# Optimization experiments

Hardware: AMD Instinct MI355X
Metric: run time of the kernel (lower is better)

The kernel has to match this reference:

```python
import jax, jax.numpy as jnp
import numpy as np

B, C, IMG = 512, 3, 112


def setup_inputs() -> dict:
    key = jax.random.key(0)
    k0, k1, k2 = jax.random.split(key, 3)
    img = jax.random.normal(k0, (B, C, IMG, IMG), dtype=jnp.float32)
    # fc[0]: Linear(3*H*W -> 20); fc[3]: Linear(20 -> 6) init weight=0, bias=identity.
    # Use small random W2 so the warp is non-trivial (math identical regardless).
    W1 = jax.random.normal(k1, (C * IMG * IMG, 20), dtype=jnp.float32) * 0.005
    b1 = jnp.zeros((20,), dtype=jnp.float32)
    W2 = jax.random.normal(k2, (20, 6), dtype=jnp.float32) * 0.01
    b2 = jnp.array([1, 0, 0, 0, 1, 0], dtype=jnp.float32)
    return {"img": img, "W1": W1, "b1": b1, "W2": W2, "b2": b2}


def reference(img, W1, b1, W2, b2):
    Bn, Cn, H, W = img.shape
    h = jnp.tanh(img.reshape(Bn, -1) @ W1 + b1)            # [B, 20]
    theta = jnp.tanh(h @ W2 + b2).reshape(Bn, 2, 3)        # [B, 2, 3]

    # F.affine_grid, align_corners=False: pixel-center normalized coords
    xs = (2.0 * jnp.arange(W, dtype=jnp.float32) + 1.0) / W - 1.0
    ys = (2.0 * jnp.arange(H, dtype=jnp.float32) + 1.0) / H - 1.0
    gy, gx = jnp.meshgrid(ys, xs, indexing="ij")           # [H, W]
    base = jnp.stack([gx, gy, jnp.ones_like(gx)], axis=-1)  # [H, W, 3] -> (x, y, 1)
    grid = jnp.einsum("bij,hwj->bhwi", theta, base)        # [B, H, W, 2], (x, y)

    # F.grid_sample, bilinear, padding_mode='zeros', align_corners=False
    ix = ((grid[..., 0] + 1.0) * W - 1.0) * 0.5            # [B, H, W] src x
    iy = ((grid[..., 1] + 1.0) * H - 1.0) * 0.5            # [B, H, W] src y
    x0f = jnp.floor(ix); y0f = jnp.floor(iy)
    wx1 = ix - x0f; wx0 = 1.0 - wx1
    wy1 = iy - y0f; wy0 = 1.0 - wy1

    img_hwc = img.transpose(0, 2, 3, 1)                    # [B, H, W, C]
    bidx = jnp.arange(Bn)[:, None, None]

    def gather(xf, yf):
        valid = (xf >= 0) & (xf <= W - 1) & (yf >= 0) & (yf <= H - 1)
        xc = jnp.clip(xf, 0, W - 1).astype(jnp.int32)
        yc = jnp.clip(yf, 0, H - 1).astype(jnp.int32)
        v = img_hwc[bidx, yc, xc]                           # [B, H, W, C]
        return v * valid[..., None].astype(img.dtype)

    out = (gather(x0f, y0f) * (wx0 * wy0)[..., None]
           + gather(x0f + 1, y0f) * (wx1 * wy0)[..., None]
           + gather(x0f, y0f + 1) * (wx0 * wy1)[..., None]
           + gather(x0f + 1, y0f + 1) * (wx1 * wy1)[..., None])
    return out.transpose(0, 3, 1, 2)                       # [B, C, H, W]
```

## Files before the change

### kernel.cpp

```cpp
#include <hip/hip_runtime.h>
#include <math.h>

#define BATCH 512
#define CHAN 3
#define IMG 112
#define HW (IMG*IMG)
#define K_TOT (CHAN*HW)
#define NH 20
#define F4_TOT (K_TOT/4)
#define KT 4
#define F4_PER_TILE (F4_TOT/KT)
#define MB 4

__global__ __launch_bounds__(256, 2)
void gemm1_kernel(const float* __restrict__ img, const float* __restrict__ W1,
                  float* __restrict__ partial) {
    const int tid = threadIdx.x;
    const int kt  = blockIdx.x;
    const int b0  = blockIdx.y * MB;
    const long base = (long)b0 * K_TOT;

    float acc[MB][NH];
    #pragma unroll
    for (int i = 0; i < MB; ++i)
        #pragma unroll
        for (int n = 0; n < NH; ++n) acc[i][n] = 0.f;

    const int f4start = kt * F4_PER_TILE;
    const int f4end   = f4start + F4_PER_TILE;

    for (int f = f4start + tid; f < f4end; f += 256) {
        const int k = f * 4;
        float4 iv[MB];
        #pragma unroll
        for (int i = 0; i < MB; ++i)
            iv[i] = *reinterpret_cast<const float4*>(img + base + (long)i * K_TOT + k);

        #pragma unroll
        for (int j = 0; j < 4; ++j) {
            const float4* wr = reinterpret_cast<const float4*>(W1 + (long)(k + j) * NH);
            float4 wq[5];
            #pragma unroll
            for (int q = 0; q < 5; ++q) wq[q] = wr[q];
            const float* wf = reinterpret_cast<const float*>(wq);
            #pragma unroll
            for (int i = 0; i < MB; ++i) {
                const float xi = reinterpret_cast<const float*>(&iv[i])[j];
                #pragma unroll
                for (int n = 0; n < NH; ++n)
                    acc[i][n] = fmaf(xi, wf[n], acc[i][n]);
            }
        }
    }

    __shared__ float red[4][MB * NH];
    const int wave = tid >> 6, lane = tid & 63;
    #pragma unroll
    for (int i = 0; i < MB; ++i)
        #pragma unroll
        for (int n = 0; n < NH; ++n) {
            float v = acc[i][n];
            #pragma unroll
            for (int off = 32; off > 0; off >>= 1) v += __shfl_xor(v, off, 64);
            if (lane == 0) red[wave][i * NH + n] = v;
        }
    __syncthreads();
    if (tid < MB * NH) {
        float s = red[0][tid] + red[1][tid] + red[2][tid] + red[3][tid];
        const int i = tid / NH, n = tid - i * NH;
        partial[((long)kt * BATCH + (b0 + i)) * NH + n] = s;
    }
}

__global__ __launch_bounds__(256)
void theta_kernel(const float* __restrict__ partial, const float* __restrict__ b1,
                  const float* __restrict__ W2, const float* __restrict__ b2,
                  float* __restrict__ theta) {
    const int b = blockIdx.x * 256 + threadIdx.x;
    if (b >= BATCH) return;
    float h[NH];
    #pragma unroll
    for (int n = 0; n < NH; ++n) {
        float s = b1[n];
        #pragma unroll
        for (int kt = 0; kt < KT; ++kt)
            s += partial[((long)kt * BATCH + b) * NH + n];
        h[n] = tanhf(s);
    }
    #pragma unroll
    for (int j = 0; j < 6; ++j) {
        float s = b2[j];
        #pragma unroll
        for (int n = 0; n < NH; ++n) s = fmaf(h[n], W2[n * 6 + j], s);
        theta[b * 6 + j] = tanhf(s);
    }
}

__global__ __launch_bounds__(256)
void warp_kernel(const float* __restrict__ img, const float* __restrict__ theta,
                 float* __restrict__ out) {
    const int b   = blockIdx.y;
    const int pix = blockIdx.x * 256 + threadIdx.x;
    const int y = pix / IMG;
    const int x = pix - y * IMG;

    const float* t = theta + b * 6;
    const float xs = (2.f * x + 1.f) / (float)IMG - 1.f;
    const float ys = (2.f * y + 1.f) / (float)IMG - 1.f;
    const float gx = t[0] * xs + t[1] * ys + t[2];
    const float gy = t[3] * xs + t[4] * ys + t[5];

    const float ix = ((gx + 1.f) * (float)IMG - 1.f) * 0.5f;
    const float iy = ((gy + 1.f) * (float)IMG - 1.f) * 0.5f;

    const float x0f = floorf(ix), y0f = floorf(iy);
    const float wx1 = ix - x0f, wx0 = 1.f - wx1;
    const float wy1 = iy - y0f, wy0 = 1.f - wy1;
    const int x0 = (int)x0f, y0 = (int)y0f;
    const int x1 = x0 + 1, y1 = y0 + 1;

    const bool vx0 = (x0 >= 0) & (x0 <= IMG - 1);
    const bool vx1 = (x1 >= 0) & (x1 <= IMG - 1);
    const bool vy0 = (y0 >= 0) & (y0 <= IMG - 1);
    const bool vy1 = (y1 >= 0) & (y1 <= IMG - 1);
    const int cx0 = min(max(x0, 0), IMG - 1), cx1 = min(max(x1, 0), IMG - 1);
    const int cy0 = min(max(y0, 0), IMG - 1), cy1 = min(max(y1, 0), IMG - 1);

    const float w00 = (vx0 && vy0) ? wx0 * wy0 : 0.f;
    const float w10 = (vx1 && vy0) ? wx1 * wy0 : 0.f;
    const float w01 = (vx0 && vy1) ? wx0 * wy1 : 0.f;
    const float w11 = (vx1 && vy1) ? wx1 * wy1 : 0.f;

    const long ib = (long)b * CHAN * HW;
    const int o00 = cy0 * IMG + cx0, o10 = cy0 * IMG + cx1;
    const int o01 = cy1 * IMG + cx0, o11 = cy1 * IMG + cx1;
    #pragma unroll
    for (int c = 0; c < CHAN; ++c) {
        const float* p = img + ib + (long)c * HW;
        const float v = w00 * p[o00] + w10 * p[o10] + w01 * p[o01] + w11 * p[o11];
        out[ib + (long)c * HW + pix] = v;
    }
}

extern "C" void kernel_launch(void* const* d_in, const int* in_sizes, int n_in,
                              void* d_out, int out_size, void* d_ws, size_t ws_size,
                              hipStream_t stream) {
    const float* img = (const float*)d_in[0];
    const float* W1  = (const float*)d_in[1];
    const float* b1  = (const float*)d_in[2];
    const float* W2  = (const float*)d_in[3];
    const float* b2  = (const float*)d_in[4];
    float* out = (float*)d_out;

    float* partial = (float*)d_ws;
    float* theta   = partial + (long)KT * BATCH * NH;

    gemm1_kernel<<<dim3(KT, BATCH / MB), 256, 0, stream>>>(img, W1, partial);
    theta_kernel<<<dim3((BATCH + 255) / 256), 256, 0, stream>>>(partial, b1, W2, b2, theta);
    warp_kernel<<<dim3(HW / 256, BATCH), 256, 0, stream>>>(img, theta, out);
}
```

Baseline: 235.4 us.

## Split GEMM K into more tiles, parallelize theta per batch, vectorize warp output

The first GEMM splits K into 16 tiles instead of 4, so the grid has four times as many blocks, and the min-blocks launch bound is dropped. The theta kernel now uses one block per batch item, with threads spread over the hidden units and outputs and a shared-memory handoff between the two layers. The warp kernel has each thread compute four adjacent pixels and write them as float4 stores, which cuts thread count and store instructions. The costs are more partial sums to reduce and more registers per warp thread.

```diff
diff --git a/kernel.cpp b/kernel.cpp
--- a/kernel.cpp
+++ b/kernel.cpp
@@ -8,11 +8,11 @@
 #define K_TOT (CHAN*HW)
 #define NH 20
 #define F4_TOT (K_TOT/4)
-#define KT 4
+#define KT 16
 #define F4_PER_TILE (F4_TOT/KT)
 #define MB 4
 
-__global__ __launch_bounds__(256, 2)
+__global__ __launch_bounds__(256)
 void gemm1_kernel(const float* __restrict__ img, const float* __restrict__ W1,
                   float* __restrict__ partial) {
     const int tid = threadIdx.x;
@@ -72,73 +72,87 @@
     }
 }
 
-__global__ __launch_bounds__(256)
+__global__ __launch_bounds__(64)
 void theta_kernel(const float* __restrict__ partial, const float* __restrict__ b1,
                   const float* __restrict__ W2, const float* __restrict__ b2,
                   float* __restrict__ theta) {
-    const int b = blockIdx.x * 256 + threadIdx.x;
-    if (b >= BATCH) return;
-    float h[NH];
-    #pragma unroll
-    for (int n = 0; n < NH; ++n) {
-        float s = b1[n];
+    const int b = blockIdx.x;
+    const int t = threadIdx.x;
+    __shared__ float h[NH];
+    if (t < NH) {
+        float s = b1[t];
         #pragma unroll
         for (int kt = 0; kt < KT; ++kt)
-            s += partial[((long)kt * BATCH + b) * NH + n];
-        h[n] = tanhf(s);
+            s += partial[((long)kt * BATCH + b) * NH + t];
+        h[t] = tanhf(s);
     }
-    #pragma unroll
-    for (int j = 0; j < 6; ++j) {
-        float s = b2[j];
+    __syncthreads();
+    if (t < 6) {
+        float s = b2[t];
         #pragma unroll
-        for (int n = 0; n < NH; ++n) s = fmaf(h[n], W2[n * 6 + j], s);
-        theta[b * 6 + j] = tanhf(s);
+        for (int n = 0; n < NH; ++n) s = fmaf(h[n], W2[n * 6 + t], s);
+        theta[b * 6 + t] = tanhf(s);
     }
 }
 
+#define QUADS (HW/4)
 __global__ __launch_bounds__(256)
 void warp_kernel(const float* __restrict__ img, const float* __restrict__ theta,
                  float* __restrict__ out) {
-    const int b   = blockIdx.y;
-    const int pix = blockIdx.x * 256 + threadIdx.x;
-    const int y = pix / IMG;
-    const int x = pix - y * IMG;
+    const int b = blockIdx.y;
+    const int quad = blockIdx.x * 256 + threadIdx.x;
+    if (quad >= QUADS) return;
+    const int y  = quad / (IMG / 4);
+    const int x0 = (quad - y * (IMG / 4)) * 4;
 
     const float* t = theta + b * 6;
-    const float xs = (2.f * x + 1.f) / (float)IMG - 1.f;
+    const float t0 = t[0], t1 = t[1], t2 = t[2], t3 = t[3], t4 = t[4], t5 = t[5];
     const float ys = (2.f * y + 1.f) / (float)IMG - 1.f;
-    const float gx = t[0] * xs + t[1] * ys + t[2];
-    const float gy = t[3] * xs + t[4] * ys + t[5];
-
-    const float ix = ((gx + 1.f) * (float)IMG - 1.f) * 0.5f;
-    const float iy = ((gy + 1.f) * (float)IMG - 1.f) * 0.5f;
-
-    const float x0f = floorf(ix), y0f = floorf(iy);
-    const float wx1 = ix - x0f, wx0 = 1.f - wx1;
-    const float wy1 = iy - y0f, wy0 = 1.f - wy1;
-    const int x0 = (int)x0f, y0 = (int)y0f;
-    const int x1 = x0 + 1, y1 = y0 + 1;
-
-    const bool vx0 = (x0 >= 0) & (x0 <= IMG - 1);
-    const bool vx1 = (x1 >= 0) & (x1 <= IMG - 1);
-    const bool vy0 = (y0 >= 0) & (y0 <= IMG - 1);
-    const bool vy1 = (y1 >= 0) & (y1 <= IMG - 1);
-    const int cx0 = min(max(x0, 0), IMG - 1), cx1 = min(max(x1, 0), IMG - 1);
-    const int cy0 = min(max(y0, 0), IMG - 1), cy1 = min(max(y1, 0), IMG - 1);
-
-    const float w00 = (vx0 && vy0) ? wx0 * wy0 : 0.f;
-    const float w10 = (vx1 && vy0) ? wx1 * wy0 : 0.f;
-    const float w01 = (vx0 && vy1) ? wx0 * wy1 : 0.f;
-    const float w11 = (vx1 && vy1) ? wx1 * wy1 : 0.f;
 
     const long ib = (long)b * CHAN * HW;
-    const int o00 = cy0 * IMG + cx0, o10 = cy0 * IMG + cx1;
-    const int o01 = cy1 * IMG + cx0, o11 = cy1 * IMG + cx1;
+    float res[CHAN][4];
+
+    #pragma unroll
+    for (int i = 0; i < 4; ++i) {
+        const float xs = (2.f * (x0 + i) + 1.f) / (float)IMG - 1.f;
+        const float gx = t0 * xs + t1 * ys + t2;
+        const float gy = t3 * xs + t4 * ys + t5;
+
+        const float ix = ((gx + 1.f) * (float)IMG - 1.f) * 0.5f;
+        const float iy = ((gy + 1.f) * (float)IMG - 1.f) * 0.5f;
+
+        const float x0f = floorf(ix), y0f = floorf(iy);
+        const float wx1 = ix - x0f, wx0 = 1.f - wx1;
+        const float wy1 = iy - y0f, wy0 = 1.f - wy1;
+        const int sx0 = (int)x0f, sy0 = (int)y0f;
+        const int sx1 = sx0 + 1, sy1 = sy0 + 1;
+
+        const bool vx0 = (sx0 >= 0) & (sx0 <= IMG - 1);
+        const bool vx1 = (sx1 >= 0) & (sx1 <= IMG - 1);
+        const bool vy0 = (sy0 >= 0) & (sy0 <= IMG - 1);
+        const bool vy1 = (sy1 >= 0) & (sy1 <= IMG - 1);
+        const int cx0 = min(max(sx0, 0), IMG - 1), cx1 = min(max(sx1, 0), IMG - 1);
+        const int cy0 = min(max(sy0, 0), IMG - 1), cy1 = min(max(sy1, 0), IMG - 1);
+
+        const float w00 = (vx0 && vy0) ? wx0 * wy0 : 0.f;
+        const float w10 = (vx1 && vy0) ? wx1 * wy0 : 0.f;
+        const float w01 = (vx0 && vy1) ? wx0 * wy1 : 0.f;
+        const float w11 = (vx1 && vy1) ? wx1 * wy1 : 0.f;
+
+        const int o00 = cy0 * IMG + cx0, o10 = cy0 * IMG + cx1;
+        const int o01 = cy1 * IMG + cx0, o11 = cy1 * IMG + cx1;
+        #pragma unroll
+        for (int c = 0; c < CHAN; ++c) {
+            const float* p = img + ib + (long)c * HW;
+            res[c][i] = w00 * p[o00] + w10 * p[o10] + w01 * p[o01] + w11 * p[o11];
+        }
+    }
+
+    const int pix0 = y * IMG + x0;
     #pragma unroll
     for (int c = 0; c < CHAN; ++c) {
-        const float* p = img + ib + (long)c * HW;
-        const float v = w00 * p[o00] + w10 * p[o10] + w01 * p[o01] + w11 * p[o11];
-        out[ib + (long)c * HW + pix] = v;
+        float4 v = make_float4(res[c][0], res[c][1], res[c][2], res[c][3]);
+        *reinterpret_cast<float4*>(out + ib + (long)c * HW + pix0) = v;
     }
 }
 
@@ -156,6 +170,6 @@
     float* theta   = partial + (long)KT * BATCH * NH;
 
     gemm1_kernel<<<dim3(KT, BATCH / MB), 256, 0, stream>>>(img, W1, partial);
-    theta_kernel<<<dim3((BATCH + 255) / 256), 256, 0, stream>>>(partial, b1, W2, b2, theta);
-    warp_kernel<<<dim3(HW / 256, BATCH), 256, 0, stream>>>(img, theta, out);
+    theta_kernel<<<dim3(BATCH), 64, 0, stream>>>(partial, b1, W2, b2, theta);
+    warp_kernel<<<dim3((QUADS + 255) / 256, BATCH), 256, 0, stream>>>(img, theta, out);
 }
```

Result: slower. 256.8 us (+9.0%).
